# Kernel tuning notes

Measured on AMD Instinct MI355X. Metric: run time of the kernel, lower is better.

The kernel has to match this reference:

```python
import jax, jax.numpy as jnp
import numpy as np

B, P, D, T = 4096, 19000, 4000, 32
H1, H2 = 2048, 1024
DIN = 2 * P + 2


def setup_inputs() -> dict:
    key = jax.random.key(0)
    ks = jax.random.split(key, 9)
    drug_pairs = jax.random.randint(ks[0], (B, 2), 0, D)
    drug_targets = jax.random.randint(ks[1], (D, T), 0, P)
    conc = jax.random.uniform(ks[2], (B, 2), dtype=jnp.float32)
    s = lambda n: 1.0 / np.sqrt(n).astype(np.float32)
    W1 = jax.random.normal(ks[3], (DIN, H1), dtype=jnp.float32) * s(DIN)
    b1 = jnp.zeros((H1,), jnp.float32)
    W2 = jax.random.normal(ks[4], (H1, H2), dtype=jnp.float32) * s(H1)
    b2 = jnp.zeros((H2,), jnp.float32)
    W3 = jax.random.normal(ks[5], (H2, 1), dtype=jnp.float32) * s(H2)
    b3 = jnp.zeros((1,), jnp.float32)
    return {"drug_pairs": drug_pairs, "drug_targets": drug_targets, "conc": conc,
            "W1": W1, "b1": b1, "W2": W2, "b2": b2, "W3": W3, "b3": b3}


def _multi_hot(drug_ids, drug_targets):
    # drug_ids: [B]; gather per-drug target lists [B, T], scatter 1s into [B, P]
    tgt = drug_targets[drug_ids]  # [B, T]
    rows = jnp.arange(drug_ids.shape[0])[:, None]
    return jnp.zeros((drug_ids.shape[0], P), jnp.float32).at[rows, tgt].set(1.0)


def reference(drug_pairs, drug_targets, conc, W1, b1, W2, b2, W3, b3):
    prot_1 = _multi_hot(drug_pairs[:, 0], drug_targets)  # [B, P]
    prot_2 = _multi_hot(drug_pairs[:, 1], drug_targets)  # [B, P]
    data_1 = jnp.concatenate([prot_1, conc[:, 0:1]], axis=1)  # [B, P+1]
    data_2 = jnp.concatenate([prot_2, conc[:, 1:2]], axis=1)
    order_1 = jnp.concatenate([data_1, data_2], axis=1)  # [B, 2P+2]
    order_2 = jnp.concatenate([data_2, data_1], axis=1)

    def mlp(x):
        h = jax.nn.relu(x @ W1 + b1)
        h = jax.nn.relu(h @ W2 + b2)
        return h @ W3 + b3

    return (mlp(order_1)[:, 0], mlp(order_2)[:, 0])
```

## Files before the change

kernel.cpp:

```cpp
#include <hip/hip_runtime.h>
#include <stdint.h>

#define B_N  4096
#define P_N  19000
#define D_N  4000
#define T_N  32
#define H1_N 2048
#define H2_N 1024

typedef __bf16 bf16x8 __attribute__((ext_vector_type(8)));
typedef float  f32x4  __attribute__((ext_vector_type(4)));

__device__ __forceinline__ unsigned short f2bf(float f) {
  union { float f; uint32_t u; } v; v.f = f;
  uint32_t u = v.u;
  uint32_t r = (u + 0x7fffu + ((u >> 16) & 1u)) >> 16;
  return (unsigned short)r;
}

__device__ __forceinline__ float bflo(uint32_t u) {
  union { uint32_t u; float f; } v; v.u = u << 16; return v.f;
}
__device__ __forceinline__ float bfhi(uint32_t u) {
  union { uint32_t u; float f; } v; v.u = u & 0xffff0000u; return v.f;
}

__device__ __forceinline__ void gload16(const void* g, void* l) {
  __builtin_amdgcn_global_load_lds((const __attribute__((address_space(1))) void*)g,
                                   (__attribute__((address_space(3))) void*)l,
                                   16, 0, 0);
}

__global__ __launch_bounds__(256) void k_setflags(const int* __restrict__ dp,
                                                  unsigned char* __restrict__ flags) {
  const int tid = threadIdx.x;
  for (int i = tid; i < D_N; i += 256) flags[i] = 0;
  __syncthreads();
  for (int i = tid; i < 2 * B_N; i += 256) flags[dp[i]] = 1;
}

__global__ __launch_bounds__(256) void k_conv(const float* __restrict__ W1,
                                              unsigned short* __restrict__ W1b) {
  const size_t base = (size_t)blockIdx.x * H1_N + threadIdx.x * 8;
  const float4* p = (const float4*)(W1 + base);
  float4 x = p[0], y = p[1];
  unsigned short r[8] = { f2bf(x.x), f2bf(x.y), f2bf(x.z), f2bf(x.w),
                          f2bf(y.x), f2bf(y.y), f2bf(y.z), f2bf(y.w) };
  *(uint4*)(W1b + base) = *(uint4*)r;
}

__global__ __launch_bounds__(256) void k_dsum(const int* __restrict__ dt,
                                              const unsigned char* __restrict__ flags,
                                              const unsigned short* __restrict__ W1b,
                                              unsigned short* __restrict__ SAb,
                                              unsigned short* __restrict__ SBb) {
  const int d = blockIdx.x;
  if (!flags[d]) return;
  __shared__ int   tgt[T_N];
  __shared__ float wgt[T_N];
  const int tid = threadIdx.x;
  if (tid < T_N) tgt[tid] = dt[d * T_N + tid];
  __syncthreads();
  if (tid < T_N) {
    int v = 1, t = tgt[tid];
    for (int j = 0; j < tid; ++j) v &= (tgt[j] != t);
    wgt[tid] = (float)v;
  }
  __syncthreads();
  const int c0 = tid * 8;
  float aA[8] = {0,0,0,0,0,0,0,0};
  float aB[8] = {0,0,0,0,0,0,0,0};
  #pragma unroll 4
  for (int t = 0; t < T_N; ++t) {
    const float  w   = wgt[t];
    const size_t row = (size_t)tgt[t];
    uint4 a = *(const uint4*)(W1b + row * H1_N + c0);
    uint4 b = *(const uint4*)(W1b + (19001 + row) * H1_N + c0);
    uint32_t au[4] = {a.x, a.y, a.z, a.w};
    uint32_t bu[4] = {b.x, b.y, b.z, b.w};
    #pragma unroll
    for (int k = 0; k < 4; ++k) {
      aA[2*k]   = fmaf(w, bflo(au[k]), aA[2*k]);
      aA[2*k+1] = fmaf(w, bfhi(au[k]), aA[2*k+1]);
      aB[2*k]   = fmaf(w, bflo(bu[k]), aB[2*k]);
      aB[2*k+1] = fmaf(w, bfhi(bu[k]), aB[2*k+1]);
    }
  }
  unsigned short oa[8], ob[8];
  #pragma unroll
  for (int k = 0; k < 8; ++k) { oa[k] = f2bf(aA[k]); ob[k] = f2bf(aB[k]); }
  *(uint4*)(SAb + (size_t)d * H1_N + c0) = *(uint4*)oa;
  *(uint4*)(SBb + (size_t)d * H1_N + c0) = *(uint4*)ob;
}

__global__ __launch_bounds__(256) void k_w2t(const float* __restrict__ W2, unsigned short* __restrict__ W2T) {
  __shared__ float tile[32][33];
  const int bx = blockIdx.x & 31;
  const int by = blockIdx.x >> 5;
  const int tx = threadIdx.x & 31, ty = threadIdx.x >> 5;
  #pragma unroll
  for (int i = 0; i < 4; ++i)
    tile[ty + i*8][tx] = W2[(size_t)(by*32 + ty + i*8) * H2_N + bx*32 + tx];
  __syncthreads();
  #pragma unroll
  for (int i = 0; i < 4; ++i) {
    const int n = bx*32 + ty + i*8;
    const int k = by*32 + tx;
    W2T[(size_t)n * H1_N + k] = f2bf(tile[tx][ty + i*8]);
  }
}

__global__ __launch_bounds__(256) void k_h1(const int* __restrict__ dp, const float* __restrict__ conc,
                                            const float* __restrict__ W1, const float* __restrict__ b1,
                                            const unsigned short* __restrict__ SAb,
                                            const unsigned short* __restrict__ SBb,
                                            unsigned short* __restrict__ h1) {
  const int rI   = blockIdx.x;
  const int swap = (rI >= B_N) ? 1 : 0;
  const int rr   = swap ? rI - B_N : rI;
  const int dA = dp[2*rr + swap];
  const int dB = dp[2*rr + (1 - swap)];
  const float cA = conc[2*rr + swap];
  const float cB = conc[2*rr + (1 - swap)];
  const int c0 = threadIdx.x * 8;
  uint4 ua = *(const uint4*)(SAb + (size_t)dA * H1_N + c0);
  uint4 ub = *(const uint4*)(SBb + (size_t)dB * H1_N + c0);
  uint32_t au[4] = {ua.x, ua.y, ua.z, ua.w};
  uint32_t bu[4] = {ub.x, ub.y, ub.z, ub.w};
  const float4* wp = (const float4*)(W1 + (size_t)P_N * H1_N + c0);
  const float4* wq = (const float4*)(W1 + (size_t)(2*P_N + 1) * H1_N + c0);
  const float4* bp = (const float4*)(b1 + c0);
  float a[8], b[8], p[8], q[8], z[8];
  #pragma unroll
  for (int k = 0; k < 4; ++k) {
    a[2*k] = bflo(au[k]); a[2*k+1] = bfhi(au[k]);
    b[2*k] = bflo(bu[k]); b[2*k+1] = bfhi(bu[k]);
  }
  float4 p0 = wp[0], p1 = wp[1], q0 = wq[0], q1 = wq[1], z0 = bp[0], z1 = bp[1];
  p[0]=p0.x;p[1]=p0.y;p[2]=p0.z;p[3]=p0.w;p[4]=p1.x;p[5]=p1.y;p[6]=p1.z;p[7]=p1.w;
  q[0]=q0.x;q[1]=q0.y;q[2]=q0.z;q[3]=q0.w;q[4]=q1.x;q[5]=q1.y;q[6]=q1.z;q[7]=q1.w;
  z[0]=z0.x;z[1]=z0.y;z[2]=z0.z;z[3]=z0.w;z[4]=z1.x;z[5]=z1.y;z[6]=z1.z;z[7]=z1.w;
  unsigned short res[8];
  #pragma unroll
  for (int k = 0; k < 8; ++k)
    res[k] = f2bf(fmaxf(a[k] + b[k] + cA*p[k] + cB*q[k] + z[k], 0.f));
  *(uint4*)(h1 + (size_t)rI * H1_N + c0) = *(uint4*)res;
}

__global__ __launch_bounds__(256) void k_gemm(const unsigned short* __restrict__ A,
                                              const unsigned short* __restrict__ Bm,
                                              const float* __restrict__ b2,
                                              const float* __restrict__ W3,
                                              float* __restrict__ partial) {
  __shared__ unsigned short As[128 * 64];
  __shared__ unsigned short Bs[128 * 64];
  __shared__ float ps[128];
  const int tid  = threadIdx.x;
  const int wv   = tid >> 6;
  const int lane = tid & 63;
  const int m0 = (blockIdx.x >> 3) * 128;
  const int n0 = (blockIdx.x & 7) * 128;
  const int wm = (wv >> 1) * 64;
  const int wn = (wv & 1) * 64;
  const int r = lane & 15;
  const int g = lane >> 4;
  const int srow = lane >> 3;
  const int slot = (lane & 7) ^ srow;

  f32x4 acc[4][4] = {};

  for (int kt = 0; kt < H1_N / 64; ++kt) {
    const int k0 = kt * 64;
    #pragma unroll
    for (int i = 0; i < 4; ++i) {
      const int c   = i * 4 + wv;
      const int row = c * 8 + srow;
      gload16(A  + (size_t)(m0 + row) * H1_N + k0 + slot * 8, (char*)As + c * 1024);
      gload16(Bm + (size_t)(n0 + row) * H1_N + k0 + slot * 8, (char*)Bs + c * 1024);
    }
    __syncthreads();
    #pragma unroll
    for (int kk = 0; kk < 2; ++kk) {
      bf16x8 af[4], bfr[4];
      #pragma unroll
      for (int mi = 0; mi < 4; ++mi) {
        const int row = wm + mi * 16 + r;
        const int s   = (kk * 4 + g) ^ (row & 7);
        af[mi] = *(const bf16x8*)((const char*)As + row * 128 + s * 16);
      }
      #pragma unroll
      for (int ni = 0; ni < 4; ++ni) {
        const int col = wn + ni * 16 + r;
        const int s   = (kk * 4 + g) ^ (col & 7);
        bfr[ni] = *(const bf16x8*)((const char*)Bs + col * 128 + s * 16);
      }
      #pragma unroll
      for (int mi = 0; mi < 4; ++mi)
        #pragma unroll
        for (int ni = 0; ni < 4; ++ni)
          acc[mi][ni] = __builtin_amdgcn_mfma_f32_16x16x32_bf16(af[mi], bfr[ni], acc[mi][ni], 0, 0, 0);
    }
    __syncthreads();
  }
  float b2v[4], w3v[4];
  #pragma unroll
  for (int ni = 0; ni < 4; ++ni) {
    const int col = n0 + wn + ni * 16 + r;
    b2v[ni] = b2[col];
    w3v[ni] = W3[col];
  }
  float rs[16];
  #pragma unroll
  for (int mi = 0; mi < 4; ++mi)
    #pragma unroll
    for (int q = 0; q < 4; ++q) {
      float s = 0.f;
      #pragma unroll
      for (int ni = 0; ni < 4; ++ni)
        s += fmaxf(acc[mi][ni][q] + b2v[ni], 0.f) * w3v[ni];
      rs[mi*4+q] = s;
    }
  #pragma unroll
  for (int o = 1; o < 16; o <<= 1)
    #pragma unroll
    for (int k = 0; k < 16; ++k)
      rs[k] += __shfl_xor(rs[k], o, 64);
  if ((wv & 1) == 0) {
    if (r == 0)
      #pragma unroll
      for (int mi = 0; mi < 4; ++mi)
        #pragma unroll
        for (int q = 0; q < 4; ++q)
          ps[wm + mi*16 + g*4 + q] = rs[mi*4+q];
  }
  __syncthreads();
  if ((wv & 1) == 1) {
    if (r == 0)
      #pragma unroll
      for (int mi = 0; mi < 4; ++mi)
        #pragma unroll
        for (int q = 0; q < 4; ++q) {
          const int rw = wm + mi*16 + g*4 + q;
          partial[(size_t)(blockIdx.x & 7) * (2*B_N) + m0 + rw] = ps[rw] + rs[mi*4+q];
        }
  }
}

__global__ __launch_bounds__(256) void k_fin(const float* __restrict__ partial,
                                             const float* __restrict__ b3,
                                             float* __restrict__ out) {
  const int i = blockIdx.x * 256 + threadIdx.x;
  float s = b3[0];
  #pragma unroll
  for (int j = 0; j < 8; ++j) s += partial[(size_t)j * (2*B_N) + i];
  out[i] = s;
}

extern "C" void kernel_launch(void* const* d_in, const int* in_sizes, int n_in,
                              void* d_out, int out_size, void* d_ws, size_t ws_size,
                              hipStream_t stream) {
  const int*   dp   = (const int*)d_in[0];
  const int*   dt   = (const int*)d_in[1];
  const float* conc = (const float*)d_in[2];
  const float* W1   = (const float*)d_in[3];
  const float* b1   = (const float*)d_in[4];
  const float* W2   = (const float*)d_in[5];
  const float* b2   = (const float*)d_in[6];
  const float* W3   = (const float*)d_in[7];
  const float* b3   = (const float*)d_in[8];
  float* out = (float*)d_out;

  char* ws = (char*)d_ws;
  unsigned short* W1b   = (unsigned short*)ws;
  unsigned short* h1    = (unsigned short*)ws;
  float*          parts = (float*)(ws + 33554432);
  unsigned short* SAb   = (unsigned short*)(ws + 155656192);
  unsigned short* SBb   = (unsigned short*)(ws + 172040192);
  unsigned short* w2t   = (unsigned short*)(ws + 188424192);
  unsigned char*  flags = (unsigned char*)(ws + 192618496);

  k_setflags<<<1,     256, 0, stream>>>(dp, flags);
  k_conv    <<<38002, 256, 0, stream>>>(W1, W1b);
  k_w2t     <<<2048,  256, 0, stream>>>(W2, w2t);
  k_dsum    <<<D_N,   256, 0, stream>>>(dt, flags, W1b, SAb, SBb);
  k_h1      <<<2*B_N, 256, 0, stream>>>(dp, conc, W1, b1, SAb, SBb, h1);
  k_gemm    <<<512,   256, 0, stream>>>(h1, w2t, b2, W3, parts);
  k_fin     <<<32,    256, 0, stream>>>(parts, b3, out);
}
```

Before: 274.8 us.

## Merge prep kernels into one launch and retile GEMM to 64x256 blocks

Merges the W1 bf16 conversion, the W2 transpose and the drug-flag setup into one k_prep launch, removing two kernel launches and their gaps. The layer-2 GEMM is retiled from 128x128 to 64x256 per block with launch_bounds occupancy 2. Each wave now covers all 64 rows and its own 64 columns, so N is split into 4 quarters instead of 8 and k_fin sums 4 partials instead of 8. The new tiling changes operand reuse and LDS size and cuts partial-sum traffic, but loads more B data per block.

```diff
diff --git a/kernel.cpp b/kernel.cpp
--- a/kernel.cpp
+++ b/kernel.cpp
@@ -31,22 +31,42 @@
                                    16, 0, 0);
 }
 
-__global__ __launch_bounds__(256) void k_setflags(const int* __restrict__ dp,
-                                                  unsigned char* __restrict__ flags) {
-  const int tid = threadIdx.x;
-  for (int i = tid; i < D_N; i += 256) flags[i] = 0;
-  __syncthreads();
-  for (int i = tid; i < 2 * B_N; i += 256) flags[dp[i]] = 1;
-}
-
-__global__ __launch_bounds__(256) void k_conv(const float* __restrict__ W1,
-                                              unsigned short* __restrict__ W1b) {
-  const size_t base = (size_t)blockIdx.x * H1_N + threadIdx.x * 8;
-  const float4* p = (const float4*)(W1 + base);
-  float4 x = p[0], y = p[1];
-  unsigned short r[8] = { f2bf(x.x), f2bf(x.y), f2bf(x.z), f2bf(x.w),
-                          f2bf(y.x), f2bf(y.y), f2bf(y.z), f2bf(y.w) };
-  *(uint4*)(W1b + base) = *(uint4*)r;
+__global__ __launch_bounds__(256) void k_prep(const float* __restrict__ W1,
+                                              unsigned short* __restrict__ W1b,
+                                              const float* __restrict__ W2,
+                                              unsigned short* __restrict__ W2T,
+                                              const int* __restrict__ dp,
+                                              unsigned char* __restrict__ flags) {
+  __shared__ float tile[32][33];
+  const int b = blockIdx.x;
+  if (b < 38002) {
+    const size_t base = (size_t)b * H1_N + threadIdx.x * 8;
+    const float4* p = (const float4*)(W1 + base);
+    float4 x = p[0], y = p[1];
+    unsigned short r[8] = { f2bf(x.x), f2bf(x.y), f2bf(x.z), f2bf(x.w),
+                            f2bf(y.x), f2bf(y.y), f2bf(y.z), f2bf(y.w) };
+    *(uint4*)(W1b + base) = *(uint4*)r;
+  } else if (b < 38002 + 2048) {
+    const int bb = b - 38002;
+    const int bx = bb & 31;
+    const int by = bb >> 5;
+    const int tx = threadIdx.x & 31, ty = threadIdx.x >> 5;
+    #pragma unroll
+    for (int i = 0; i < 4; ++i)
+      tile[ty + i*8][tx] = W2[(size_t)(by*32 + ty + i*8) * H2_N + bx*32 + tx];
+    __syncthreads();
+    #pragma unroll
+    for (int i = 0; i < 4; ++i) {
+      const int n = bx*32 + ty + i*8;
+      const int k = by*32 + tx;
+      W2T[(size_t)n * H1_N + k] = f2bf(tile[tx][ty + i*8]);
+    }
+  } else {
+    const int tid = threadIdx.x;
+    for (int i = tid; i < D_N; i += 256) flags[i] = 0;
+    __syncthreads();
+    for (int i = tid; i < 2 * B_N; i += 256) flags[dp[i]] = 1;
+  }
 }
 
 __global__ __launch_bounds__(256) void k_dsum(const int* __restrict__ dt,
@@ -91,23 +111,6 @@
   for (int k = 0; k < 8; ++k) { oa[k] = f2bf(aA[k]); ob[k] = f2bf(aB[k]); }
   *(uint4*)(SAb + (size_t)d * H1_N + c0) = *(uint4*)oa;
   *(uint4*)(SBb + (size_t)d * H1_N + c0) = *(uint4*)ob;
-}
-
-__global__ __launch_bounds__(256) void k_w2t(const float* __restrict__ W2, unsigned short* __restrict__ W2T) {
-  __shared__ float tile[32][33];
-  const int bx = blockIdx.x & 31;
-  const int by = blockIdx.x >> 5;
-  const int tx = threadIdx.x & 31, ty = threadIdx.x >> 5;
-  #pragma unroll
-  for (int i = 0; i < 4; ++i)
-    tile[ty + i*8][tx] = W2[(size_t)(by*32 + ty + i*8) * H2_N + bx*32 + tx];
-  __syncthreads();
-  #pragma unroll
-  for (int i = 0; i < 4; ++i) {
-    const int n = bx*32 + ty + i*8;
-    const int k = by*32 + tx;
-    W2T[(size_t)n * H1_N + k] = f2bf(tile[tx][ty + i*8]);
-  }
 }
 
 __global__ __launch_bounds__(256) void k_h1(const int* __restrict__ dp, const float* __restrict__ conc,
@@ -147,21 +150,22 @@
   *(uint4*)(h1 + (size_t)rI * H1_N + c0) = *(uint4*)res;
 }
 
-__global__ __launch_bounds__(256) void k_gemm(const unsigned short* __restrict__ A,
-                                              const unsigned short* __restrict__ Bm,
-                                              const float* __restrict__ b2,
-                                              const float* __restrict__ W3,
-                                              float* __restrict__ partial) {
-  __shared__ unsigned short As[128 * 64];
-  __shared__ unsigned short Bs[128 * 64];
-  __shared__ float ps[128];
+__global__ __launch_bounds__(256, 2) void k_gemm(const unsigned short* __restrict__ A,
+                                                 const unsigned short* __restrict__ Bm,
+                                                 const float* __restrict__ b2,
+                                                 const float* __restrict__ W3,
+                                                 float* __restrict__ partial) {
+  __shared__ unsigned short As[64 * 64];
+  __shared__ unsigned short Bs[256 * 64];
+  __shared__ float ps[4][64];
   const int tid  = threadIdx.x;
   const int wv   = tid >> 6;
   const int lane = tid & 63;
-  const int m0 = (blockIdx.x >> 3) * 128;
-  const int n0 = (blockIdx.x & 7) * 128;
-  const int wm = (wv >> 1) * 64;
-  const int wn = (wv & 1) * 64;
+  const int bid  = blockIdx.x;
+  const int m0 = (bid >> 2) * 64;
+  const int nq = bid & 3;
+  const int n0 = nq * 256;
+  const int wn = wv * 64;
   const int r = lane & 15;
   const int g = lane >> 4;
   const int srow = lane >> 3;
@@ -169,13 +173,18 @@
 
   f32x4 acc[4][4] = {};
 
-  for (int kt = 0; kt < H1_N / 64; ++kt) {
+  for (int kt = 0; kt < 32; ++kt) {
     const int k0 = kt * 64;
     #pragma unroll
-    for (int i = 0; i < 4; ++i) {
+    for (int i = 0; i < 2; ++i) {
       const int c   = i * 4 + wv;
       const int row = c * 8 + srow;
-      gload16(A  + (size_t)(m0 + row) * H1_N + k0 + slot * 8, (char*)As + c * 1024);
+      gload16(A + (size_t)(m0 + row) * H1_N + k0 + slot * 8, (char*)As + c * 1024);
+    }
+    #pragma unroll
+    for (int i = 0; i < 8; ++i) {
+      const int c   = i * 4 + wv;
+      const int row = c * 8 + srow;
       gload16(Bm + (size_t)(n0 + row) * H1_N + k0 + slot * 8, (char*)Bs + c * 1024);
     }
     __syncthreads();
@@ -184,7 +193,7 @@
       bf16x8 af[4], bfr[4];
       #pragma unroll
       for (int mi = 0; mi < 4; ++mi) {
-        const int row = wm + mi * 16 + r;
+        const int row = mi * 16 + r;
         const int s   = (kk * 4 + g) ^ (row & 7);
         af[mi] = *(const bf16x8*)((const char*)As + row * 128 + s * 16);
       }
@@ -225,25 +234,16 @@
     #pragma unroll
     for (int k = 0; k < 16; ++k)
       rs[k] += __shfl_xor(rs[k], o, 64);
-  if ((wv & 1) == 0) {
-    if (r == 0)
-      #pragma unroll
-      for (int mi = 0; mi < 4; ++mi)
-        #pragma unroll
-        for (int q = 0; q < 4; ++q)
-          ps[wm + mi*16 + g*4 + q] = rs[mi*4+q];
-  }
+  if (r == 0)
+    #pragma unroll
+    for (int mi = 0; mi < 4; ++mi)
+      #pragma unroll
+      for (int q = 0; q < 4; ++q)
+        ps[wv][mi*16 + g*4 + q] = rs[mi*4+q];
   __syncthreads();
-  if ((wv & 1) == 1) {
-    if (r == 0)
-      #pragma unroll
-      for (int mi = 0; mi < 4; ++mi)
-        #pragma unroll
-        for (int q = 0; q < 4; ++q) {
-          const int rw = wm + mi*16 + g*4 + q;
-          partial[(size_t)(blockIdx.x & 7) * (2*B_N) + m0 + rw] = ps[rw] + rs[mi*4+q];
-        }
-  }
+  if (tid < 64)
+    partial[(size_t)nq * (2*B_N) + m0 + tid] =
+        ps[0][tid] + ps[1][tid] + ps[2][tid] + ps[3][tid];
 }
 
 __global__ __launch_bounds__(256) void k_fin(const float* __restrict__ partial,
@@ -252,7 +252,7 @@
   const int i = blockIdx.x * 256 + threadIdx.x;
   float s = b3[0];
   #pragma unroll
-  for (int j = 0; j < 8; ++j) s += partial[(size_t)j * (2*B_N) + i];
+  for (int j = 0; j < 4; ++j) s += partial[(size_t)j * (2*B_N) + i];
   out[i] = s;
 }
 
@@ -279,11 +279,9 @@
   unsigned short* w2t   = (unsigned short*)(ws + 188424192);
   unsigned char*  flags = (unsigned char*)(ws + 192618496);
 
-  k_setflags<<<1,     256, 0, stream>>>(dp, flags);
-  k_conv    <<<38002, 256, 0, stream>>>(W1, W1b);
-  k_w2t     <<<2048,  256, 0, stream>>>(W2, w2t);
-  k_dsum    <<<D_N,   256, 0, stream>>>(dt, flags, W1b, SAb, SBb);
-  k_h1      <<<2*B_N, 256, 0, stream>>>(dp, conc, W1, b1, SAb, SBb, h1);
-  k_gemm    <<<512,   256, 0, stream>>>(h1, w2t, b2, W3, parts);
-  k_fin     <<<32,    256, 0, stream>>>(parts, b3, out);
-}
+  k_prep<<<40051,  256, 0, stream>>>(W1, W1b, W2, w2t, dp, flags);
+  k_dsum<<<D_N,    256, 0, stream>>>(dt, flags, W1b, SAb, SBb);
+  k_h1  <<<2*B_N,  256, 0, stream>>>(dp, conc, W1, b1, SAb, SBb, h1);
+  k_gemm<<<512,    256, 0, stream>>>(h1, w2t, b2, W3, parts);
+  k_fin <<<32,     256, 0, stream>>>(parts, b3, out);
+}
```

After: 267.8 us. 2.5% less time.
